# Kernel optimization log

Hardware: AMD Instinct MI355X
Metric: run time of the kernel (lower is better)

## Reference

```python
import jax, jax.numpy as jnp
import numpy as np

HIDDEN = 1024  # must match init_kwargs hidden_size


def setup_inputs() -> dict:
    key = jax.random.key(0)
    k1, k2 = jax.random.split(key)
    B, SQ, SKV, D = 4, 4096, 4096, HIDDEN
    query = jax.random.normal(k1, (B, SQ, D), dtype=jnp.float32)
    key_value_states = jax.random.normal(k2, (B, SKV, D), dtype=jnp.float32)
    attention_mask = jnp.zeros((B, 1, SKV), dtype=jnp.float32)
    return {
        "query": query,
        "key_value_states": key_value_states,
        "attention_mask": attention_mask,
        "layer_idx": 0,
    }


def reference(query, key_value_states, attention_mask, layer_idx):
    # compression_rate = 1.0 + layer_idx/12*3 ; layer_idx=0 -> rate 1.0 (no compression)
    scale = 1.0 / jnp.sqrt(jnp.asarray(HIDDEN, dtype=query.dtype))
    # scores: [B, Sq, Skv]
    scores = jnp.einsum("bqd,bkd->bqk", query, key_value_states) * scale
    scores = scores + attention_mask
    attn = jax.nn.softmax(scores, axis=-1)
    # dropout is identity (eval / p=0)
    out = jnp.einsum("bqk,bkd->bqd", attn, key_value_states)
    return out, attn
```

## Files before the change

kernel.cpp:

```cpp
#include <hip/hip_runtime.h>
#include <hip/hip_fp16.h>
#include <stdint.h>

#define B_   4
#define SQ_  4096
#define SKV_ 4096
#define D_   1024

typedef __attribute__((ext_vector_type(4))) float f32x4;
typedef __attribute__((ext_vector_type(8))) short bf8_t;

__device__ __forceinline__ unsigned short f2bf(float f) {
    unsigned u = __float_as_uint(f);
    u += 0x7fff + ((u >> 16) & 1);
    return (unsigned short)(u >> 16);
}

__device__ __forceinline__ void gload_lds16(const void* g, void* l) {
    __builtin_amdgcn_global_load_lds(
        (const __attribute__((address_space(1))) unsigned int*)g,
        (__attribute__((address_space(3))) unsigned int*)l,
        16, 0, 0);
}

__device__ __forceinline__ void barrier_mem() {
    asm volatile("" ::: "memory");
    __builtin_amdgcn_s_barrier();
    asm volatile("" ::: "memory");
}

__global__ void cvt_f32_bf16_kernel(const float* __restrict__ in,
                                    unsigned short* __restrict__ out, int n4) {
    int stride = gridDim.x * blockDim.x;
    for (int i = blockIdx.x * blockDim.x + threadIdx.x; i < n4; i += stride) {
        float4 v = ((const float4*)in)[i];
        ushort4 o;
        o.x = f2bf(v.x); o.y = f2bf(v.y); o.z = f2bf(v.z); o.w = f2bf(v.w);
        ((ushort4*)out)[i] = o;
    }
}

__global__ void cvtkv_kernel(const float* __restrict__ V,
                             unsigned short* __restrict__ Kbf,
                             unsigned short* __restrict__ VT) {
    __shared__ float tile[32][33];
    int b = blockIdx.z;
    const float* Vb = V + (size_t)b * SKV_ * D_;
    unsigned short* Kb = Kbf + (size_t)b * SKV_ * D_;
    unsigned short* VTb = VT + (size_t)b * D_ * SKV_;
    int d0 = blockIdx.x * 32, k0 = blockIdx.y * 32;
    int x = threadIdx.x, y = threadIdx.y;
    #pragma unroll
    for (int i = 0; i < 4; ++i) {
        float v = Vb[(size_t)(k0 + y + i * 8) * D_ + d0 + x];
        tile[y + i * 8][x] = v;
        Kb[(size_t)(k0 + y + i * 8) * D_ + d0 + x] = f2bf(v);
    }
    __syncthreads();
    #pragma unroll
    for (int i = 0; i < 4; ++i)
        VTb[(size_t)(d0 + y + i * 8) * SKV_ + k0 + x] = f2bf(tile[x][y + i * 8]);
}

template<bool HALF_OUT>
__global__ __launch_bounds__(512, 2) void gemm256_pipe_kernel(
    const unsigned short* __restrict__ A, int lda, size_t strideA,
    const unsigned short* __restrict__ Bm, int ldb, size_t strideB,
    void* __restrict__ Cv, int ldc, size_t strideC,
    int K, float scale, const float* __restrict__ mask)
{
    __shared__ __align__(16) unsigned char smem[131072];

    const int tid  = threadIdx.x;
    const int lane = tid & 63, wid = tid >> 6;
    const int wr = wid >> 2, wc = wid & 3;

    int lin  = blockIdx.y * gridDim.x + blockIdx.x;
    int q8   = (gridDim.x * gridDim.y) >> 3;
    int lin2 = (lin & 7) * q8 + (lin >> 3);
    int bn = lin2 % gridDim.x, bm = lin2 / gridDim.x;
    int bz = blockIdx.z;

    const char* Ab = (const char*)(A + (size_t)bz * strideA);
    const char* Bb = (const char*)(Bm + (size_t)bz * strideB);
    const int ldaB = lda * 2, ldbB = ldb * 2;

    const int srow = ((tid >> 6) * 16) + (tid & 15);
    const int scol = ((tid >> 4) & 3) * 16;
    const char* Apan = Ab + (size_t)(bm * 256 + srow) * ldaB + scol;
    const char* Bpan = Bb + (size_t)(bn * 256 + srow) * ldbB + scol;
    char* ldsA = (char*)smem;
    char* ldsB = (char*)smem + 65536;

    const char* aRd = (char*)smem + wr * 8192 + lane * 16;
    const char* bRd = (char*)smem + 65536 + wc * 4096 + lane * 16;

    f32x4 acc[8][4] = {};
    const int NT = K >> 6;

#define STAGE_A(tt, hh) do { \
    const char* s_ = Apan + (tt) * 128 + (hh) * 64; \
    char* d_ = ldsA + (((tt) & 1) * 32768) + (hh) * 16384 + tid * 16; \
    gload_lds16(s_, d_); \
    gload_lds16(s_ + (size_t)128 * ldaB, d_ + 8192); \
} while (0)
#define STAGE_B(tt, hh) do { \
    const char* s_ = Bpan + (tt) * 128 + (hh) * 64; \
    char* d_ = ldsB + (((tt) & 1) * 32768) + (hh) * 16384 + tid * 16; \
    gload_lds16(s_, d_); \
    gload_lds16(s_ + (size_t)128 * ldbB, d_ + 8192); \
} while (0)
#define MFMA16(ACCBASE, AF, BF) do { \
    __builtin_amdgcn_s_setprio(1); \
    _Pragma("unroll") \
    for (int m_ = 0; m_ < 4; ++m_) \
        _Pragma("unroll") \
        for (int n_ = 0; n_ < 4; ++n_) \
            acc[(ACCBASE) + m_][n_] = __builtin_amdgcn_mfma_f32_16x16x32_bf16( \
                AF[m_], BF[n_], acc[(ACCBASE) + m_][n_], 0, 0, 0); \
    __builtin_amdgcn_s_setprio(0); \
} while (0)

    STAGE_B(0, 0); STAGE_A(0, 0); STAGE_B(0, 1); STAGE_A(0, 1);
    if (NT > 1) {
        STAGE_B(1, 0); STAGE_A(1, 0); STAGE_B(1, 1);
        asm volatile("s_waitcnt vmcnt(10)" ::: "memory");
    } else {
        asm volatile("s_waitcnt vmcnt(0)" ::: "memory");
    }
    barrier_mem();

    bf8_t aL[4], aH[4], bA[4], bB[4];
    #pragma unroll
    for (int m = 0; m < 4; ++m) aL[m] = *(const bf8_t*)(aRd + m * 1024);
    #pragma unroll
    for (int n = 0; n < 4; ++n) bA[n] = *(const bf8_t*)(bRd + n * 1024);

    for (int t = 0; t < NT; ++t) {
        const int p = t & 1;
        const char* aT = aRd + p * 32768;
        const char* bT = bRd + p * 32768;

        if (t + 1 < NT) STAGE_A(t + 1, 1);
        barrier_mem();
        #pragma unroll
        for (int m = 0; m < 4; ++m) aH[m] = *(const bf8_t*)(aT + (4 + m) * 1024);
        MFMA16(0, aL, bA);
        barrier_mem();

        if (t == NT - 1) asm volatile("s_waitcnt vmcnt(0)" ::: "memory");
        else             asm volatile("s_waitcnt vmcnt(8)" ::: "memory");
        if (t + 2 < NT) STAGE_B(t + 2, 0);
        barrier_mem();
        #pragma unroll
        for (int m = 0; m < 4; ++m) aL[m] = *(const bf8_t*)(aT + 16384 + m * 1024);
        #pragma unroll
        for (int n = 0; n < 4; ++n) bB[n] = *(const bf8_t*)(bT + 16384 + n * 1024);
        MFMA16(4, aH, bA);
        barrier_mem();

        if (t + 2 < NT) STAGE_A(t + 2, 0);
        barrier_mem();
        #pragma unroll
        for (int m = 0; m < 4; ++m) aH[m] = *(const bf8_t*)(aT + 16384 + (4 + m) * 1024);
        MFMA16(0, aL, bB);
        barrier_mem();

        if (t + 2 < NT) {
            asm volatile("s_waitcnt vmcnt(8)" ::: "memory");
            STAGE_B(t + 2, 1);
        } else if (t + 1 < NT) {
            asm volatile("s_waitcnt vmcnt(4)" ::: "memory");
        }
        barrier_mem();
        if (t + 1 < NT) {
            const char* aTn = aRd + (p ^ 1) * 32768;
            const char* bTn = bRd + (p ^ 1) * 32768;
            #pragma unroll
            for (int m = 0; m < 4; ++m) aL[m] = *(const bf8_t*)(aTn + m * 1024);
            #pragma unroll
            for (int n = 0; n < 4; ++n) bA[n] = *(const bf8_t*)(bTn + n * 1024);
        }
        MFMA16(4, aH, bB);
        barrier_mem();
    }
#undef STAGE_A
#undef STAGE_B
#undef MFMA16

    const int row0 = bm * 256 + wr * 128 + (lane >> 4) * 4;
    const int col0 = bn * 256 + wc * 64 + (lane & 15);
    if (HALF_OUT) {
        __half* Ch = (__half*)Cv + (size_t)bz * strideC;
        const float* maskb = mask + (size_t)bz * SKV_;
        #pragma unroll
        for (int n = 0; n < 4; ++n) {
            int col = col0 + n * 16;
            float mk = maskb[col];
            #pragma unroll
            for (int m = 0; m < 8; ++m) {
                int row = row0 + m * 16;
                #pragma unroll
                for (int r = 0; r < 4; ++r)
                    Ch[(size_t)(row + r) * ldc + col] = __float2half(acc[m][n][r] * scale + mk);
            }
        }
    } else {
        float* Cf = (float*)Cv + (size_t)bz * strideC;
        #pragma unroll
        for (int n = 0; n < 4; ++n) {
            int col = col0 + n * 16;
            #pragma unroll
            for (int m = 0; m < 8; ++m) {
                int row = row0 + m * 16;
                #pragma unroll
                for (int r = 0; r < 4; ++r)
                    Cf[(size_t)(row + r) * ldc + col] = acc[m][n][r];
            }
        }
    }
}

__global__ __launch_bounds__(256) void softmax_kernel(unsigned short* __restrict__ s2,
                                                      float* __restrict__ attn) {
    __shared__ __align__(16) float buf[SKV_];
    __shared__ float red[4];
    size_t row = blockIdx.x;
    unsigned short* p = s2 + row * SKV_;
    float* ao = attn + row * SKV_;
    int t = threadIdx.x;

    float lmax = -3.4e38f;
    for (int i = t * 8; i < SKV_; i += 2048) {
        uint4 hv = *(const uint4*)(p + i);
        float2 f0 = __half22float2(*(__half2*)&hv.x);
        float2 f1 = __half22float2(*(__half2*)&hv.y);
        float2 f2 = __half22float2(*(__half2*)&hv.z);
        float2 f3 = __half22float2(*(__half2*)&hv.w);
        buf[i+0] = f0.x; buf[i+1] = f0.y; buf[i+2] = f1.x; buf[i+3] = f1.y;
        buf[i+4] = f2.x; buf[i+5] = f2.y; buf[i+6] = f3.x; buf[i+7] = f3.y;
        lmax = fmaxf(lmax, fmaxf(fmaxf(fmaxf(f0.x, f0.y), fmaxf(f1.x, f1.y)),
                                 fmaxf(fmaxf(f2.x, f2.y), fmaxf(f3.x, f3.y))));
    }
    #pragma unroll
    for (int o = 32; o; o >>= 1) lmax = fmaxf(lmax, __shfl_down(lmax, o));
    if ((t & 63) == 0) red[t >> 6] = lmax;
    __syncthreads();
    float rmax = fmaxf(fmaxf(red[0], red[1]), fmaxf(red[2], red[3]));
    __syncthreads();

    float lsum = 0.f;
    for (int i = t * 4; i < SKV_; i += 1024) {
        float4 v = *(const float4*)&buf[i];
        v.x = __expf(v.x - rmax); v.y = __expf(v.y - rmax);
        v.z = __expf(v.z - rmax); v.w = __expf(v.w - rmax);
        *(float4*)&buf[i] = v;
        lsum += (v.x + v.y) + (v.z + v.w);
    }
    #pragma unroll
    for (int o = 32; o; o >>= 1) lsum += __shfl_down(lsum, o);
    if ((t & 63) == 0) red[t >> 6] = lsum;
    __syncthreads();
    float rinv = 1.0f / ((red[0] + red[1]) + (red[2] + red[3]));

    for (int i = t * 8; i < SKV_; i += 2048) {
        float4 v0 = *(const float4*)&buf[i];
        float4 v1 = *(const float4*)&buf[i + 4];
        v0.x *= rinv; v0.y *= rinv; v0.z *= rinv; v0.w *= rinv;
        v1.x *= rinv; v1.y *= rinv; v1.z *= rinv; v1.w *= rinv;
        *(float4*)(ao + i) = v0;
        *(float4*)(ao + i + 4) = v1;
        ushort4 o0, o1;
        o0.x = f2bf(v0.x); o0.y = f2bf(v0.y); o0.z = f2bf(v0.z); o0.w = f2bf(v0.w);
        o1.x = f2bf(v1.x); o1.y = f2bf(v1.y); o1.z = f2bf(v1.z); o1.w = f2bf(v1.w);
        *(ushort4*)(p + i) = o0;
        *(ushort4*)(p + i + 4) = o1;
    }
}

__global__ __launch_bounds__(256) void softmax_f32_kernel(float* __restrict__ scores) {
    __shared__ __align__(16) float buf[SKV_];
    __shared__ float red[4];
    size_t row = blockIdx.x;
    float* p = scores + row * SKV_;
    int t = threadIdx.x;
    float lmax = -3.4e38f;
    for (int i = t * 4; i < SKV_; i += 1024) {
        float4 v = *(const float4*)(p + i);
        *(float4*)&buf[i] = v;
        lmax = fmaxf(fmaxf(lmax, fmaxf(v.x, v.y)), fmaxf(v.z, v.w));
    }
    #pragma unroll
    for (int o = 32; o; o >>= 1) lmax = fmaxf(lmax, __shfl_down(lmax, o));
    if ((t & 63) == 0) red[t >> 6] = lmax;
    __syncthreads();
    float rmax = fmaxf(fmaxf(red[0], red[1]), fmaxf(red[2], red[3]));
    __syncthreads();
    float lsum = 0.f;
    for (int i = t * 4; i < SKV_; i += 1024) {
        float4 v = *(const float4*)&buf[i];
        v.x = __expf(v.x - rmax); v.y = __expf(v.y - rmax);
        v.z = __expf(v.z - rmax); v.w = __expf(v.w - rmax);
        *(float4*)&buf[i] = v;
        lsum += (v.x + v.y) + (v.z + v.w);
    }
    #pragma unroll
    for (int o = 32; o; o >>= 1) lsum += __shfl_down(lsum, o);
    if ((t & 63) == 0) red[t >> 6] = lsum;
    __syncthreads();
    float rinv = 1.0f / ((red[0] + red[1]) + (red[2] + red[3]));
    for (int i = t * 4; i < SKV_; i += 1024) {
        float4 v = *(const float4*)&buf[i];
        v.x *= rinv; v.y *= rinv; v.z *= rinv; v.w *= rinv;
        *(float4*)(p + i) = v;
    }
}

__global__ void naive_nt_kernel(const float* __restrict__ A, const float* __restrict__ Bm,
                                float* __restrict__ C, const float* __restrict__ mask,
                                int N, int K, float scale) {
    __shared__ float As[16][16], Bs[16][16];
    int b = blockIdx.z;
    const float* Ab = A + (size_t)b * SQ_ * K;
    const float* Bb = Bm + (size_t)b * N * K;
    float* Cb = C + (size_t)b * SQ_ * N;
    int tx = threadIdx.x, ty = threadIdx.y;
    int m = blockIdx.y * 16 + ty, n = blockIdx.x * 16 + tx;
    float acc = 0.f;
    for (int k0 = 0; k0 < K; k0 += 16) {
        As[ty][tx] = Ab[(size_t)m * K + k0 + tx];
        Bs[ty][tx] = Bb[(size_t)(blockIdx.x * 16 + ty) * K + k0 + tx];
        __syncthreads();
        #pragma unroll
        for (int kk = 0; kk < 16; ++kk) acc += As[ty][kk] * Bs[tx][kk];
        __syncthreads();
    }
    Cb[(size_t)m * N + n] = acc * scale + (mask ? mask[(size_t)b * SKV_ + n] : 0.f);
}

__global__ void naive_nn_kernel(const float* __restrict__ A, const float* __restrict__ Bm,
                                float* __restrict__ C, int N, int K) {
    __shared__ float As[16][16], Bs[16][17];
    int b = blockIdx.z;
    const float* Ab = A + (size_t)b * SQ_ * K;
    const float* Bb = Bm + (size_t)b * K * N;
    float* Cb = C + (size_t)b * SQ_ * N;
    int tx = threadIdx.x, ty = threadIdx.y;
    int m = blockIdx.y * 16 + ty, n = blockIdx.x * 16 + tx;
    float acc = 0.f;
    for (int k0 = 0; k0 < K; k0 += 16) {
        As[ty][tx] = Ab[(size_t)m * K + k0 + tx];
        Bs[ty][tx] = Bb[(size_t)(k0 + ty) * N + n];
        __syncthreads();
        #pragma unroll
        for (int kk = 0; kk < 16; ++kk) acc += As[ty][kk] * Bs[kk][tx];
        __syncthreads();
    }
    Cb[(size_t)m * N + n] = acc;
}

extern "C" void kernel_launch(void* const* d_in, const int* in_sizes, int n_in,
                              void* d_out, int out_size, void* d_ws, size_t ws_size,
                              hipStream_t stream) {
    const float* q    = (const float*)d_in[0];
    const float* kv   = (const float*)d_in[1];
    const float* mask = (const float*)d_in[2];

    float* out  = (float*)d_out;
    float* attn = out + (size_t)B_ * SQ_ * D_;
    const float scale = 0.03125f;

    size_t nQ    = (size_t)B_ * SQ_ * D_;
    size_t nKV   = (size_t)B_ * SKV_ * D_;
    size_t nAttn = (size_t)B_ * SQ_ * SKV_;
    size_t need  = (nQ + nKV + nKV + nAttn) * 2;

    if (ws_size >= need) {
        unsigned short* qbf  = (unsigned short*)d_ws;
        unsigned short* kbf  = qbf + nQ;
        unsigned short* vtbf = kbf + nKV;
        unsigned short* s2   = vtbf + nKV;

        cvt_f32_bf16_kernel<<<2048, 256, 0, stream>>>(q, qbf, (int)(nQ / 4));
        cvtkv_kernel<<<dim3(D_ / 32, SKV_ / 32, B_), dim3(32, 8), 0, stream>>>(kv, kbf, vtbf);

        gemm256_pipe_kernel<true><<<dim3(SKV_ / 256, SQ_ / 256, B_), 512, 0, stream>>>(
            qbf, D_, (size_t)SQ_ * D_,
            kbf, D_, (size_t)SKV_ * D_,
            (void*)s2, SKV_, (size_t)SQ_ * SKV_,
            D_, scale, mask);

        softmax_kernel<<<B_ * SQ_, 256, 0, stream>>>(s2, attn);

        gemm256_pipe_kernel<false><<<dim3(D_ / 256, SQ_ / 256, B_), 512, 0, stream>>>(
            s2, SKV_, (size_t)SQ_ * SKV_,
            vtbf, SKV_, (size_t)D_ * SKV_,
            (void*)out, D_, (size_t)SQ_ * D_,
            SKV_, 1.0f, nullptr);
    } else {
        naive_nt_kernel<<<dim3(SKV_ / 16, SQ_ / 16, B_), dim3(16, 16), 0, stream>>>(
            q, kv, attn, mask, SKV_, D_, scale);
        softmax_f32_kernel<<<B_ * SQ_, 256, 0, stream>>>(attn);
        naive_nn_kernel<<<dim3(D_ / 16, SQ_ / 16, B_), dim3(16, 16), 0, stream>>>(
            attn, kv, out, D_, SKV_);
    }
}
```

Baseline: 482.8 us.

## Replace 256x256 pipelined GEMM with simpler 128x128 single-buffered GEMM

Swaps the hand-pipelined 256x256-tile, 512-thread, double-buffered bf16 MFMA GEMM for a 128x128-tile, 256-thread kernel with one LDS buffer and a plain load-sync-compute loop. Smaller tiles and LDS use are meant to raise occupancy and block count, letting the scheduler hide latency instead of explicit software pipelining. In exchange each tile gets less reuse, global traffic grows, and loads no longer overlap with MFMA work inside a block.

```diff
diff --git a/kernel.cpp b/kernel.cpp
--- a/kernel.cpp
+++ b/kernel.cpp
@@ -21,12 +21,6 @@
         (const __attribute__((address_space(1))) unsigned int*)g,
         (__attribute__((address_space(3))) unsigned int*)l,
         16, 0, 0);
-}
-
-__device__ __forceinline__ void barrier_mem() {
-    asm volatile("" ::: "memory");
-    __builtin_amdgcn_s_barrier();
-    asm volatile("" ::: "memory");
 }
 
 __global__ void cvt_f32_bf16_kernel(const float* __restrict__ in,
@@ -63,17 +57,17 @@
 }
 
 template<bool HALF_OUT>
-__global__ __launch_bounds__(512, 2) void gemm256_pipe_kernel(
+__global__ __launch_bounds__(256, 3) void gemm128_kernel(
     const unsigned short* __restrict__ A, int lda, size_t strideA,
     const unsigned short* __restrict__ Bm, int ldb, size_t strideB,
     void* __restrict__ Cv, int ldc, size_t strideC,
     int K, float scale, const float* __restrict__ mask)
 {
-    __shared__ __align__(16) unsigned char smem[131072];
+    __shared__ __align__(16) unsigned char smem[32768];
 
     const int tid  = threadIdx.x;
     const int lane = tid & 63, wid = tid >> 6;
-    const int wr = wid >> 2, wc = wid & 3;
+    const int wr = wid >> 1, wc = wid & 1;
 
     int lin  = blockIdx.y * gridDim.x + blockIdx.x;
     int q8   = (gridDim.x * gridDim.y) >> 3;
@@ -85,111 +79,51 @@
     const char* Bb = (const char*)(Bm + (size_t)bz * strideB);
     const int ldaB = lda * 2, ldbB = ldb * 2;
 
-    const int srow = ((tid >> 6) * 16) + (tid & 15);
-    const int scol = ((tid >> 4) & 3) * 16;
-    const char* Apan = Ab + (size_t)(bm * 256 + srow) * ldaB + scol;
-    const char* Bpan = Bb + (size_t)(bn * 256 + srow) * ldbB + scol;
+    const char* aSrc[4]; const char* bSrc[4]; int dstOff[4];
+    #pragma unroll
+    for (int q = 0; q < 4; ++q) {
+        int o = q * 256 + tid;
+        int g = o & 3, r = (o >> 2) & 127, kk = o >> 9;
+        aSrc[q] = Ab + (size_t)(bm * 128 + r) * ldaB + kk * 64 + g * 16;
+        bSrc[q] = Bb + (size_t)(bn * 128 + r) * ldbB + kk * 64 + g * 16;
+        dstOff[q] = o * 16;
+    }
     char* ldsA = (char*)smem;
-    char* ldsB = (char*)smem + 65536;
-
-    const char* aRd = (char*)smem + wr * 8192 + lane * 16;
-    const char* bRd = (char*)smem + 65536 + wc * 4096 + lane * 16;
-
-    f32x4 acc[8][4] = {};
-    const int NT = K >> 6;
-
-#define STAGE_A(tt, hh) do { \
-    const char* s_ = Apan + (tt) * 128 + (hh) * 64; \
-    char* d_ = ldsA + (((tt) & 1) * 32768) + (hh) * 16384 + tid * 16; \
-    gload_lds16(s_, d_); \
-    gload_lds16(s_ + (size_t)128 * ldaB, d_ + 8192); \
-} while (0)
-#define STAGE_B(tt, hh) do { \
-    const char* s_ = Bpan + (tt) * 128 + (hh) * 64; \
-    char* d_ = ldsB + (((tt) & 1) * 32768) + (hh) * 16384 + tid * 16; \
-    gload_lds16(s_, d_); \
-    gload_lds16(s_ + (size_t)128 * ldbB, d_ + 8192); \
-} while (0)
-#define MFMA16(ACCBASE, AF, BF) do { \
-    __builtin_amdgcn_s_setprio(1); \
-    _Pragma("unroll") \
-    for (int m_ = 0; m_ < 4; ++m_) \
-        _Pragma("unroll") \
-        for (int n_ = 0; n_ < 4; ++n_) \
-            acc[(ACCBASE) + m_][n_] = __builtin_amdgcn_mfma_f32_16x16x32_bf16( \
-                AF[m_], BF[n_], acc[(ACCBASE) + m_][n_], 0, 0, 0); \
-    __builtin_amdgcn_s_setprio(0); \
-} while (0)
-
-    STAGE_B(0, 0); STAGE_A(0, 0); STAGE_B(0, 1); STAGE_A(0, 1);
-    if (NT > 1) {
-        STAGE_B(1, 0); STAGE_A(1, 0); STAGE_B(1, 1);
-        asm volatile("s_waitcnt vmcnt(10)" ::: "memory");
-    } else {
-        asm volatile("s_waitcnt vmcnt(0)" ::: "memory");
-    }
-    barrier_mem();
-
-    bf8_t aL[4], aH[4], bA[4], bB[4];
-    #pragma unroll
-    for (int m = 0; m < 4; ++m) aL[m] = *(const bf8_t*)(aRd + m * 1024);
-    #pragma unroll
-    for (int n = 0; n < 4; ++n) bA[n] = *(const bf8_t*)(bRd + n * 1024);
-
-    for (int t = 0; t < NT; ++t) {
-        const int p = t & 1;
-        const char* aT = aRd + p * 32768;
-        const char* bT = bRd + p * 32768;
-
-        if (t + 1 < NT) STAGE_A(t + 1, 1);
-        barrier_mem();
-        #pragma unroll
-        for (int m = 0; m < 4; ++m) aH[m] = *(const bf8_t*)(aT + (4 + m) * 1024);
-        MFMA16(0, aL, bA);
-        barrier_mem();
-
-        if (t == NT - 1) asm volatile("s_waitcnt vmcnt(0)" ::: "memory");
-        else             asm volatile("s_waitcnt vmcnt(8)" ::: "memory");
-        if (t + 2 < NT) STAGE_B(t + 2, 0);
-        barrier_mem();
-        #pragma unroll
-        for (int m = 0; m < 4; ++m) aL[m] = *(const bf8_t*)(aT + 16384 + m * 1024);
-        #pragma unroll
-        for (int n = 0; n < 4; ++n) bB[n] = *(const bf8_t*)(bT + 16384 + n * 1024);
-        MFMA16(4, aH, bA);
-        barrier_mem();
-
-        if (t + 2 < NT) STAGE_A(t + 2, 0);
-        barrier_mem();
-        #pragma unroll
-        for (int m = 0; m < 4; ++m) aH[m] = *(const bf8_t*)(aT + 16384 + (4 + m) * 1024);
-        MFMA16(0, aL, bB);
-        barrier_mem();
-
-        if (t + 2 < NT) {
-            asm volatile("s_waitcnt vmcnt(8)" ::: "memory");
-            STAGE_B(t + 2, 1);
-        } else if (t + 1 < NT) {
-            asm volatile("s_waitcnt vmcnt(4)" ::: "memory");
+    char* ldsB = (char*)smem + 16384;
+
+    const int rbase = (lane & 15) * 64 + (lane >> 4) * 16;
+    const char* aRd = ldsA + wr * 4096 + rbase;
+    const char* bRd = ldsB + wc * 4096 + rbase;
+
+    f32x4 acc[4][4] = {};
+
+    for (int k0 = 0; k0 < K; k0 += 64) {
+        #pragma unroll
+        for (int q = 0; q < 4; ++q) gload_lds16(aSrc[q], ldsA + dstOff[q]);
+        #pragma unroll
+        for (int q = 0; q < 4; ++q) gload_lds16(bSrc[q], ldsB + dstOff[q]);
+        #pragma unroll
+        for (int q = 0; q < 4; ++q) { aSrc[q] += 128; bSrc[q] += 128; }
+        __syncthreads();
+        #pragma unroll
+        for (int kk = 0; kk < 2; ++kk) {
+            bf8_t af[4], bfv[4];
+            #pragma unroll
+            for (int m = 0; m < 4; ++m) af[m]  = *(const bf8_t*)(aRd + kk * 8192 + m * 1024);
+            #pragma unroll
+            for (int n = 0; n < 4; ++n) bfv[n] = *(const bf8_t*)(bRd + kk * 8192 + n * 1024);
+            #pragma unroll
+            for (int m = 0; m < 4; ++m)
+                #pragma unroll
+                for (int n = 0; n < 4; ++n)
+                    acc[m][n] = __builtin_amdgcn_mfma_f32_16x16x32_bf16(
+                        af[m], bfv[n], acc[m][n], 0, 0, 0);
         }
-        barrier_mem();
-        if (t + 1 < NT) {
-            const char* aTn = aRd + (p ^ 1) * 32768;
-            const char* bTn = bRd + (p ^ 1) * 32768;
-            #pragma unroll
-            for (int m = 0; m < 4; ++m) aL[m] = *(const bf8_t*)(aTn + m * 1024);
-            #pragma unroll
-            for (int n = 0; n < 4; ++n) bA[n] = *(const bf8_t*)(bTn + n * 1024);
-        }
-        MFMA16(4, aH, bB);
-        barrier_mem();
-    }
-#undef STAGE_A
-#undef STAGE_B
-#undef MFMA16
-
-    const int row0 = bm * 256 + wr * 128 + (lane >> 4) * 4;
-    const int col0 = bn * 256 + wc * 64 + (lane & 15);
+        __syncthreads();
+    }
+
+    const int row0 = bm * 128 + wr * 64 + (lane >> 4) * 4;
+    const int col0 = bn * 128 + wc * 64 + (lane & 15);
     if (HALF_OUT) {
         __half* Ch = (__half*)Cv + (size_t)bz * strideC;
         const float* maskb = mask + (size_t)bz * SKV_;
@@ -198,7 +132,7 @@
             int col = col0 + n * 16;
             float mk = maskb[col];
             #pragma unroll
-            for (int m = 0; m < 8; ++m) {
+            for (int m = 0; m < 4; ++m) {
                 int row = row0 + m * 16;
                 #pragma unroll
                 for (int r = 0; r < 4; ++r)
@@ -211,7 +145,7 @@
         for (int n = 0; n < 4; ++n) {
             int col = col0 + n * 16;
             #pragma unroll
-            for (int m = 0; m < 8; ++m) {
+            for (int m = 0; m < 4; ++m) {
                 int row = row0 + m * 16;
                 #pragma unroll
                 for (int r = 0; r < 4; ++r)
@@ -384,7 +318,7 @@
         cvt_f32_bf16_kernel<<<2048, 256, 0, stream>>>(q, qbf, (int)(nQ / 4));
         cvtkv_kernel<<<dim3(D_ / 32, SKV_ / 32, B_), dim3(32, 8), 0, stream>>>(kv, kbf, vtbf);
 
-        gemm256_pipe_kernel<true><<<dim3(SKV_ / 256, SQ_ / 256, B_), 512, 0, stream>>>(
+        gemm128_kernel<true><<<dim3(SKV_ / 128, SQ_ / 128, B_), 256, 0, stream>>>(
             qbf, D_, (size_t)SQ_ * D_,
             kbf, D_, (size_t)SKV_ * D_,
             (void*)s2, SKV_, (size_t)SQ_ * SKV_,
@@ -392,7 +326,7 @@
 
         softmax_kernel<<<B_ * SQ_, 256, 0, stream>>>(s2, attn);
 
-        gemm256_pipe_kernel<false><<<dim3(D_ / 256, SQ_ / 256, B_), 512, 0, stream>>>(
+        gemm128_kernel<false><<<dim3(D_ / 128, SQ_ / 128, B_), 256, 0, stream>>>(
             s2, SKV_, (size_t)SQ_ * SKV_,
             vtbf, SKV_, (size_t)D_ * SKV_,
             (void*)out, D_, (size_t)SQ_ * D_,
```

Result: no change. 480.9 us, median of 2 (-0.4%).
